# Performance work log

Hardware: AMD Instinct MI355X
Metric: run time of the kernel (lower is better)

Reference implementation:

```python
import jax, jax.numpy as jnp
import numpy as np

B, N, D, H = 128, 256, 256, 256
N_POWER_ITERS = 5  # matches spectral_norm(n_power_iterations=5)


def setup_inputs() -> dict:
    key = jax.random.key(0)
    ks = jax.random.split(key, 8)
    w = lambda k, shape: jax.random.normal(k, shape, dtype=jnp.float32) * 0.05
    return {
        "x": jax.random.normal(ks[0], (B, N, D), dtype=jnp.float32),
        "Wq": w(ks[1], (H, D)), "bq": w(ks[2], (H,)),
        "Wk": w(ks[3], (H, D)), "bk": w(ks[4], (H,)),
        "Wv": w(ks[5], (D, D)), "bv": w(ks[6], (D,)),
        "u0": jax.random.normal(ks[7], (D,), dtype=jnp.float32),
    }


def _l2norm(v, eps=1e-12):
    return v / (jnp.linalg.norm(v) + eps)


def _spectral_normalize(W, u0):
    # torch spectral_norm: power iteration (no grad) to get u, v; sigma = u^T W v (with grad)
    u = _l2norm(u0)
    v = _l2norm(W.T @ u)
    def body(i, uv):
        u, v = uv
        v = _l2norm(W.T @ u)
        u = _l2norm(W @ v)
        return (u, v)
    u, v = jax.lax.fori_loop(0, N_POWER_ITERS, body, (u, v))
    u = jax.lax.stop_gradient(u)
    v = jax.lax.stop_gradient(v)
    sigma = u @ (W @ v)
    return W / sigma


def reference(x, Wq, bq, Wk, bk, Wv, bv, u0):
    # torch Linear: y = x @ W.T + b, W is [out, in]
    q = jnp.einsum('bnd,hd->bnh', x, Wq) + bq          # [B, N, H]
    k = jnp.einsum('bnd,hd->bnh', x, Wk) + bk          # [B, N, H]
    Wv_sn = _spectral_normalize(Wv, u0)
    vals = jnp.einsum('bnd,od->bno', x, Wv_sn) + bv    # [B, N, D]
    scores = jnp.einsum('bnh,bmh->bnm', q, k)          # [B, N, N]
    # track_grads=False -> eigenvals detached; stop_gradient input so eig has no tangent path
    ev = jnp.linalg.eigvals(jax.lax.stop_gradient(scores))  # complex [B, N]
    rho = jnp.max(jnp.abs(ev), axis=-1)[:, None, None]      # spectral radius [B,1,1]
    attention = scores / rho
    weighted = jnp.einsum('bnm,bmd->bnd', attention, vals)  # [B, N, D]
    return weighted, attention
```

## Files before the change

kernel.cpp:

```cpp
#include <hip/hip_runtime.h>
#include <hip/hip_bf16.h>


#define NB 128
#define MAT 65536
#define BIG 8388608LL

typedef __attribute__((ext_vector_type(4))) float floatx4;
typedef __attribute__((ext_vector_type(4))) float f4v;
typedef __attribute__((ext_vector_type(8))) short short8v;
typedef __attribute__((ext_vector_type(4))) short short4v;

__device__ __forceinline__ short f2bf(float x) {
  union { float f; unsigned u; } v; v.f = x;
  unsigned r = v.u + 0x7fff + ((v.u >> 16) & 1);
  return (short)(r >> 16);
}
__device__ __forceinline__ float bf2f(short h) {
  union { unsigned u; float f; } v; v.u = ((unsigned)(unsigned short)h) << 16; return v.f;
}

template<bool TB, bool BATCHED>
__global__ __launch_bounds__(256) void gemm_mfma(
    const float* __restrict__ A, const float* __restrict__ B, float* __restrict__ C,
    long long sA, long long sB, long long sC,
    const float* __restrict__ bias,
    const float* __restrict__ scale_ptr, int sstride, int smode,
    float* __restrict__ norm_out,
    float* __restrict__ att_out,
    const float* __restrict__ B2, const float* __restrict__ bias2, float* __restrict__ C2,
    const float* __restrict__ B3, float* __restrict__ C3,
    const float* __restrict__ bsc, const float* __restrict__ bsb)
{
  __shared__ short sAhi[128 * 32], sAlo[128 * 32];
  __shared__ short sBhi[128 * 40], sBlo[128 * 40];

  int bz, m0, n0;
  if constexpr (BATCHED) {
    int lin = blockIdx.x;
    int xcd = lin & 7;
    int s = lin >> 3;
    bz = xcd * 16 + (s >> 2);
    int tile = s & 3;
    m0 = (tile >> 1) * 128;
    n0 = (tile & 1) * 128;
  } else {
    bz = 0;
    m0 = blockIdx.y * 128;
    n0 = (blockIdx.x & 1) * 128;
    int sel = blockIdx.x >> 1;
    if (sel == 1) { B = B2; bias = bias2; C = C2; }
    else if (sel == 2) { B = B3; bias = nullptr; C = C3; }
  }
  A += (long long)bz * sA;
  B += (long long)bz * sB;
  C += (long long)bz * sC;

  const int t = threadIdx.x;
  const int lane = t & 63;
  const int wave = t >> 6;
  const int wm = wave >> 1, wn = wave & 1;
  const int q = lane >> 4, c16 = lane & 15;

  float alpha = 1.0f;
  if (smode == 1) alpha = 1.0f / scale_ptr[bz * sstride];
  else if (smode == 2) alpha = scale_ptr[bz * sstride];

  float rinv_att = alpha;
  const bool do_att = (att_out != nullptr) && (n0 == 0);

  float binv = 1.0f;
  if (bsc) binv = 1.0f / bsc[0];

  floatx4 acc[4][4];
  #pragma unroll
  for (int i = 0; i < 4; i++)
    #pragma unroll
    for (int j = 0; j < 4; j++)
      acc[i][j] = (floatx4){0.f, 0.f, 0.f, 0.f};

  for (int k0 = 0; k0 < 256; k0 += 32) {
    #pragma unroll
    for (int i = 0; i < 4; i++) {
      int f = t + i * 256;
      int row = f >> 3, c4 = f & 7;
      f4v v = *(const f4v*)(A + (long long)(m0 + row) * 256 + k0 + c4 * 4);
      if (do_att)
        *(f4v*)(att_out + (long long)bz * MAT + (long long)(m0 + row) * 256 + k0 + c4 * 4)
            = v * rinv_att;
      short4v h, l;
      #pragma unroll
      for (int e = 0; e < 4; e++) {
        short hh = f2bf(v[e]);
        h[e] = hh;
        l[e] = f2bf(v[e] - bf2f(hh));
      }
      *(short4v*)&sAhi[row * 32 + c4 * 4] = h;
      *(short4v*)&sAlo[row * 32 + c4 * 4] = l;
    }
    if constexpr (TB) {
      #pragma unroll
      for (int i = 0; i < 4; i++) {
        int f = t + i * 256;
        int row = f >> 3, c4 = f & 7;
        f4v v = *(const f4v*)(B + (long long)(n0 + row) * 256 + k0 + c4 * 4);
        short4v h, l;
        #pragma unroll
        for (int e = 0; e < 4; e++) {
          short hh = f2bf(v[e]);
          h[e] = hh;
          l[e] = f2bf(v[e] - bf2f(hh));
        }
        *(short4v*)&sBhi[row * 40 + c4 * 4] = h;
        *(short4v*)&sBlo[row * 40 + c4 * 4] = l;
      }
      __syncthreads();
    } else {
      __shared__ float sT[32 * 132];
      #pragma unroll
      for (int i = 0; i < 4; i++) {
        int f = t + i * 256;
        int kk = f >> 5, n4 = f & 31;
        f4v v = *(const f4v*)(B + (long long)(k0 + kk) * 256 + n0 + n4 * 4);
        if (bsb) {
          #pragma unroll
          for (int e = 0; e < 4; e++) v[e] = v[e] * binv + bsb[n0 + n4 * 4 + e];
        }
        *(f4v*)&sT[kk * 132 + n4 * 4] = v;
      }
      __syncthreads();
      int n = t & 127, kh = t >> 7;
      short8v h0, h1, l0, l1;
      #pragma unroll
      for (int j = 0; j < 8; j++) {
        float x0 = sT[(kh * 16 + j) * 132 + n];
        float x1 = sT[(kh * 16 + 8 + j) * 132 + n];
        short a0 = f2bf(x0), a1 = f2bf(x1);
        h0[j] = a0; l0[j] = f2bf(x0 - bf2f(a0));
        h1[j] = a1; l1[j] = f2bf(x1 - bf2f(a1));
      }
      *(short8v*)&sBhi[n * 40 + kh * 16] = h0;
      *(short8v*)&sBhi[n * 40 + kh * 16 + 8] = h1;
      *(short8v*)&sBlo[n * 40 + kh * 16] = l0;
      *(short8v*)&sBlo[n * 40 + kh * 16 + 8] = l1;
      __syncthreads();
    }

    short8v ah[4], al[4], bh[4], bl[4];
    #pragma unroll
    for (int fi = 0; fi < 4; fi++) {
      int r = wm * 64 + fi * 16 + c16;
      ah[fi] = *(short8v*)&sAhi[r * 32 + q * 8];
      al[fi] = *(short8v*)&sAlo[r * 32 + q * 8];
    }
    #pragma unroll
    for (int fj = 0; fj < 4; fj++) {
      int r = wn * 64 + fj * 16 + c16;
      bh[fj] = *(short8v*)&sBhi[r * 40 + q * 8];
      bl[fj] = *(short8v*)&sBlo[r * 40 + q * 8];
    }
    #pragma unroll
    for (int fi = 0; fi < 4; fi++)
      #pragma unroll
      for (int fj = 0; fj < 4; fj++) {
        acc[fi][fj] = __builtin_amdgcn_mfma_f32_16x16x32_bf16(al[fi], bh[fj], acc[fi][fj], 0, 0, 0);
        acc[fi][fj] = __builtin_amdgcn_mfma_f32_16x16x32_bf16(ah[fi], bl[fj], acc[fi][fj], 0, 0, 0);
        acc[fi][fj] = __builtin_amdgcn_mfma_f32_16x16x32_bf16(ah[fi], bh[fj], acc[fi][fj], 0, 0, 0);
      }
    __syncthreads();
  }

  float ssq = 0.f;
  #pragma unroll
  for (int fi = 0; fi < 4; fi++) {
    #pragma unroll
    for (int fj = 0; fj < 4; fj++) {
      int col = n0 + wn * 64 + fj * 16 + c16;
      float bb = bias ? bias[col] : 0.f;
      #pragma unroll
      for (int r = 0; r < 4; r++) {
        int row = m0 + wm * 64 + fi * 16 + q * 4 + r;
        float v = acc[fi][fj][r] * alpha + bb;
        C[(long long)row * 256 + col] = v;
        ssq += v * v;
      }
    }
  }

  if (norm_out) {
    float* red = (float*)sAhi;
    red[t] = ssq;
    __syncthreads();
    for (int off = 128; off > 0; off >>= 1) {
      if (t < off) red[t] += red[t + off];
      __syncthreads();
    }
    if (t == 0) {
      int tl = ((m0 >> 7) << 1) | (n0 >> 7);
      norm_out[bz * 4 + tl] = red[0];
    }
  }
}

__global__ __launch_bounds__(256) void split_inputs(
    const float* __restrict__ Wq, const float* __restrict__ Wk,
    const float* __restrict__ Wv, short* __restrict__ ws6,
    const float* __restrict__ x, short* __restrict__ xhi, short* __restrict__ xlo)
{
  int b = blockIdx.x;
  int t = threadIdx.x;
  if (b < 192) {
    int gid = b * 256 + t;
    int m = gid >> 14;
    int off = (gid & 16383) * 4;
    const float* src = (m == 0) ? Wq : (m == 1) ? Wk : Wv;
    f4v v = *(const f4v*)(src + off);
    short4v h, l;
    #pragma unroll
    for (int e = 0; e < 4; e++) {
      short hh = f2bf(v[e]);
      h[e] = hh;
      l[e] = f2bf(v[e] - bf2f(hh));
    }
    *(short4v*)&ws6[(long long)(m * 2) * MAT + off] = h;
    *(short4v*)&ws6[(long long)(m * 2 + 1) * MAT + off] = l;
  } else {
    long long off = ((long long)(b - 192) * 256 + t) * 8;
    #pragma unroll
    for (int half = 0; half < 2; half++) {
      f4v v = *(const f4v*)(x + off + half * 4);
      short4v h, l;
      #pragma unroll
      for (int e = 0; e < 4; e++) {
        short hh = f2bf(v[e]);
        h[e] = hh;
        l[e] = f2bf(v[e] - bf2f(hh));
      }
      *(short4v*)&xhi[off + half * 4] = h;
      *(short4v*)&xlo[off + half * 4] = l;
    }
  }
}

__global__ __launch_bounds__(256) void proj_qkv(
    const short* __restrict__ xhi, const short* __restrict__ xlo,
    const short* __restrict__ wsp,
    const float* __restrict__ bq, const float* __restrict__ bk,
    short* __restrict__ qhi, short* __restrict__ qlo,
    short* __restrict__ khi, short* __restrict__ klo,
    float* __restrict__ vals)
{
  __shared__ short sAhi[128 * 32], sAlo[128 * 32];
  __shared__ short sBhi[128 * 40], sBlo[128 * 40];

  const int lin = blockIdx.x;
  const int xcd = lin & 7;
  const int idx = lin >> 3;
  const int mloc = idx / 6;
  const int s6 = idx - mloc * 6;
  const int m0 = (xcd * 32 + mloc) * 128;
  const int sel = s6 >> 1;
  const int n0 = (s6 & 1) * 128;

  const short* wb_hi = wsp + (long long)(sel * 2) * MAT;
  const short* wb_lo = wsp + (long long)(sel * 2 + 1) * MAT;

  const int t = threadIdx.x;
  const int lane = t & 63;
  const int wave = t >> 6;
  const int wm = wave >> 1, wn = wave & 1;
  const int q = lane >> 4, c16 = lane & 15;

  floatx4 acc[4][4];
  #pragma unroll
  for (int i = 0; i < 4; i++)
    #pragma unroll
    for (int j = 0; j < 4; j++)
      acc[i][j] = (floatx4){0.f, 0.f, 0.f, 0.f};

  for (int k0 = 0; k0 < 256; k0 += 32) {
    #pragma unroll
    for (int i = 0; i < 2; i++) {
      int chunk = t + i * 256;
      int row = chunk >> 2, c8 = chunk & 3;
      long long ga = (long long)(m0 + row) * 256 + k0 + c8 * 8;
      *(short8v*)&sAhi[row * 32 + c8 * 8] = *(const short8v*)(xhi + ga);
      *(short8v*)&sAlo[row * 32 + c8 * 8] = *(const short8v*)(xlo + ga);
    }
    #pragma unroll
    for (int i = 0; i < 2; i++) {
      int chunk = t + i * 256;
      int row = chunk >> 2, c8 = chunk & 3;
      long long gr = (long long)(n0 + row) * 256 + k0 + c8 * 8;
      *(short8v*)&sBhi[row * 40 + c8 * 8] = *(const short8v*)(wb_hi + gr);
      *(short8v*)&sBlo[row * 40 + c8 * 8] = *(const short8v*)(wb_lo + gr);
    }
    __syncthreads();

    short8v ah[4], al[4], bh[4], bl[4];
    #pragma unroll
    for (int fi = 0; fi < 4; fi++) {
      int r = wm * 64 + fi * 16 + c16;
      ah[fi] = *(short8v*)&sAhi[r * 32 + q * 8];
      al[fi] = *(short8v*)&sAlo[r * 32 + q * 8];
    }
    #pragma unroll
    for (int fj = 0; fj < 4; fj++) {
      int r = wn * 64 + fj * 16 + c16;
      bh[fj] = *(short8v*)&sBhi[r * 40 + q * 8];
      bl[fj] = *(short8v*)&sBlo[r * 40 + q * 8];
    }
    #pragma unroll
    for (int fi = 0; fi < 4; fi++)
      #pragma unroll
      for (int fj = 0; fj < 4; fj++) {
        acc[fi][fj] = __builtin_amdgcn_mfma_f32_16x16x32_bf16(al[fi], bh[fj], acc[fi][fj], 0, 0, 0);
        acc[fi][fj] = __builtin_amdgcn_mfma_f32_16x16x32_bf16(ah[fi], bl[fj], acc[fi][fj], 0, 0, 0);
        acc[fi][fj] = __builtin_amdgcn_mfma_f32_16x16x32_bf16(ah[fi], bh[fj], acc[fi][fj], 0, 0, 0);
      }
    __syncthreads();
  }

  if (sel < 2) {
    short* ohi = sel ? khi : qhi;
    short* olo = sel ? klo : qlo;
    const float* bb = sel ? bk : bq;
    #pragma unroll
    for (int fi = 0; fi < 4; fi++)
      #pragma unroll
      for (int fj = 0; fj < 4; fj++) {
        int col = n0 + wn * 64 + fj * 16 + c16;
        float b = bb[col];
        #pragma unroll
        for (int r = 0; r < 4; r++) {
          long long row = m0 + wm * 64 + fi * 16 + q * 4 + r;
          float v = acc[fi][fj][r] + b;
          short h = f2bf(v);
          ohi[row * 256 + col] = h;
          olo[row * 256 + col] = f2bf(v - bf2f(h));
        }
      }
  } else {
    #pragma unroll
    for (int fi = 0; fi < 4; fi++)
      #pragma unroll
      for (int fj = 0; fj < 4; fj++) {
        int col = n0 + wn * 64 + fj * 16 + c16;
        #pragma unroll
        for (int r = 0; r < 4; r++) {
          long long row = m0 + wm * 64 + fi * 16 + q * 4 + r;
          vals[row * 256 + col] = acc[fi][fj][r];
        }
      }
  }
}

__global__ __launch_bounds__(256) void scores_st(
    const short* __restrict__ qhi, const short* __restrict__ qlo,
    const short* __restrict__ khi, const short* __restrict__ klo,
    float* __restrict__ S, float* __restrict__ norm_out)
{
  __shared__ short sAhi[128 * 32], sAlo[128 * 32];
  __shared__ short sBhi[128 * 40], sBlo[128 * 40];
  __shared__ float red[256];

  const int lin = blockIdx.x;
  const int xcd = lin & 7, s = lin >> 3;
  const int bz = xcd * 16 + (s >> 2);
  const int tile = s & 3;
  const int m0 = (tile >> 1) * 128, n0 = (tile & 1) * 128;

  const int t = threadIdx.x;
  const int lane = t & 63;
  const int wave = t >> 6;
  const int wm = wave >> 1, wn = wave & 1;
  const int q = lane >> 4, c16 = lane & 15;

  floatx4 acc[4][4];
  #pragma unroll
  for (int i = 0; i < 4; i++)
    #pragma unroll
    for (int j = 0; j < 4; j++)
      acc[i][j] = (floatx4){0.f, 0.f, 0.f, 0.f};

  const long long abase = (long long)(bz * 256 + m0) * 256;
  const long long bbase = (long long)(bz * 256 + n0) * 256;

  for (int k0 = 0; k0 < 256; k0 += 32) {
    #pragma unroll
    for (int i = 0; i < 2; i++) {
      int chunk = t + i * 256;
      int row = chunk >> 2, c8 = chunk & 3;
      long long ga = abase + (long long)row * 256 + k0 + c8 * 8;
      long long gb = bbase + (long long)row * 256 + k0 + c8 * 8;
      *(short8v*)&sAhi[row * 32 + c8 * 8] = *(const short8v*)(qhi + ga);
      *(short8v*)&sAlo[row * 32 + c8 * 8] = *(const short8v*)(qlo + ga);
      *(short8v*)&sBhi[row * 40 + c8 * 8] = *(const short8v*)(khi + gb);
      *(short8v*)&sBlo[row * 40 + c8 * 8] = *(const short8v*)(klo + gb);
    }
    __syncthreads();

    short8v ah[4], al[4], bh[4], bl[4];
    #pragma unroll
    for (int fi = 0; fi < 4; fi++) {
      int r = wm * 64 + fi * 16 + c16;
      ah[fi] = *(short8v*)&sAhi[r * 32 + q * 8];
      al[fi] = *(short8v*)&sAlo[r * 32 + q * 8];
    }
    #pragma unroll
    for (int fj = 0; fj < 4; fj++) {
      int r = wn * 64 + fj * 16 + c16;
      bh[fj] = *(short8v*)&sBhi[r * 40 + q * 8];
      bl[fj] = *(short8v*)&sBlo[r * 40 + q * 8];
    }
    #pragma unroll
    for (int fi = 0; fi < 4; fi++)
      #pragma unroll
      for (int fj = 0; fj < 4; fj++) {
        acc[fi][fj] = __builtin_amdgcn_mfma_f32_16x16x32_bf16(al[fi], bh[fj], acc[fi][fj], 0, 0, 0);
        acc[fi][fj] = __builtin_amdgcn_mfma_f32_16x16x32_bf16(ah[fi], bl[fj], acc[fi][fj], 0, 0, 0);
        acc[fi][fj] = __builtin_amdgcn_mfma_f32_16x16x32_bf16(ah[fi], bh[fj], acc[fi][fj], 0, 0, 0);
      }
    __syncthreads();
  }

  float* C = S + (long long)bz * MAT;
  float ssq = 0.f;
  #pragma unroll
  for (int fi = 0; fi < 4; fi++)
    #pragma unroll
    for (int fj = 0; fj < 4; fj++) {
      int col = n0 + wn * 64 + fj * 16 + c16;
      #pragma unroll
      for (int r = 0; r < 4; r++) {
        int row = m0 + wm * 64 + fi * 16 + q * 4 + r;
        float v = acc[fi][fj][r];
        C[(long long)row * 256 + col] = v;
        ssq += v * v;
      }
    }

  red[t] = ssq;
  __syncthreads();
  for (int off = 128; off > 0; off >>= 1) {
    if (t < off) red[t] += red[t + off];
    __syncthreads();
  }
  if (t == 0) norm_out[bz * 4 + tile] = red[0];
}

__device__ __forceinline__ void chain_epilogue(
    short* LB, float* red, floatx4 (&acc)[4][4], float alpha,
    int m0, int n0, int wm, int wn, int q, int c16, int t,
    short* __restrict__ Mout,
    float* __restrict__ nout, int bz, int tile, bool write_out)
{
  __syncthreads();
  float ssq = 0.f;
  #pragma unroll
  for (int fi = 0; fi < 4; fi++)
    #pragma unroll
    for (int fj = 0; fj < 4; fj++) {
      int lcol = wn * 64 + fj * 16 + c16;
      #pragma unroll
      for (int r = 0; r < 4; r++) {
        int lrow = wm * 64 + fi * 16 + q * 4 + r;
        float v = acc[fi][fj][r] * alpha;
        ssq += v * v;
        if (write_out) LB[lrow * 128 + lcol] = f2bf(v);
      }
    }

  if (write_out) {
    __syncthreads();
    int lr = t >> 1, off = (t & 1) * 64;
    #pragma unroll
    for (int jc = 0; jc < 8; jc++)
      *(short8v*)(Mout + (long long)(m0 + lr) * 256 + n0 + off + jc * 8)
          = *(const short8v*)&LB[lr * 128 + off + jc * 8];
  }

  red[t] = ssq;
  __syncthreads();
  for (int off2 = 128; off2 > 0; off2 >>= 1) {
    if (t < off2) red[t] += red[t + off2];
    __syncthreads();
  }
  if (t == 0) nout[bz * 4 + tile] = red[0];
}

__global__ __launch_bounds__(256) void sq_f32bf(
    const float* __restrict__ S, short* __restrict__ Mo,
    const float* __restrict__ nprev, float* __restrict__ nout)
{
  __shared__ short SM[18432];
  __shared__ float sT[32 * 132];
  __shared__ float red[256];
  short* sAhi = SM;
  short* sAlo = SM + 4096;
  short* sBhi = SM + 8192;
  short* sBlo = SM + 13312;

  int lin = blockIdx.x;
  int xcd = lin & 7, s = lin >> 3;
  int bz = xcd * 16 + (s >> 2);
  int tile = s & 3;
  int m0 = (tile >> 1) * 128, n0 = (tile & 1) * 128;
  const float* A = S + (long long)bz * MAT;

  const int t = threadIdx.x;
  const int lane = t & 63;
  const int wave = t >> 6;
  const int wm = wave >> 1, wn = wave & 1;
  const int q = lane >> 4, c16 = lane & 15;

  floatx4 acc[4][4];
  #pragma unroll
  for (int i = 0; i < 4; i++)
    #pragma unroll
    for (int j = 0; j < 4; j++)
      acc[i][j] = (floatx4){0.f, 0.f, 0.f, 0.f};

  for (int k0 = 0; k0 < 256; k0 += 32) {
    #pragma unroll
    for (int i = 0; i < 4; i++) {
      int f = t + i * 256;
      int row = f >> 3, c4 = f & 7;
      f4v v = *(const f4v*)(A + (long long)(m0 + row) * 256 + k0 + c4 * 4);
      short4v h, l;
      #pragma unroll
      for (int e = 0; e < 4; e++) {
        short hh = f2bf(v[e]);
        h[e] = hh;
        l[e] = f2bf(v[e] - bf2f(hh));
      }
      *(short4v*)&sAhi[row * 32 + c4 * 4] = h;
      *(short4v*)&sAlo[row * 32 + c4 * 4] = l;
    }
    #pragma unroll
    for (int i = 0; i < 4; i++) {
      int f = t + i * 256;
      int kk = f >> 5, n4 = f & 31;
      f4v v = *(const f4v*)(A + (long long)(k0 + kk) * 256 + n0 + n4 * 4);
      *(f4v*)&sT[kk * 132 + n4 * 4] = v;
    }
    __syncthreads();
    {
      int n = t & 127, kh = t >> 7;
      short8v h0, h1, l0, l1;
      #pragma unroll
      for (int j = 0; j < 8; j++) {
        float x0 = sT[(kh * 16 + j) * 132 + n];
        float x1 = sT[(kh * 16 + 8 + j) * 132 + n];
        short a0 = f2bf(x0), a1 = f2bf(x1);
        h0[j] = a0; l0[j] = f2bf(x0 - bf2f(a0));
        h1[j] = a1; l1[j] = f2bf(x1 - bf2f(a1));
      }
      *(short8v*)&sBhi[n * 40 + kh * 16] = h0;
      *(short8v*)&sBhi[n * 40 + kh * 16 + 8] = h1;
      *(short8v*)&sBlo[n * 40 + kh * 16] = l0;
      *(short8v*)&sBlo[n * 40 + kh * 16 + 8] = l1;
    }
    __syncthreads();

    short8v ah[4], al[4], bh[4], bl[4];
    #pragma unroll
    for (int fi = 0; fi < 4; fi++) {
      int r = wm * 64 + fi * 16 + c16;
      ah[fi] = *(short8v*)&sAhi[r * 32 + q * 8];
      al[fi] = *(short8v*)&sAlo[r * 32 + q * 8];
    }
    #pragma unroll
    for (int fj = 0; fj < 4; fj++) {
      int r = wn * 64 + fj * 16 + c16;
      bh[fj] = *(short8v*)&sBhi[r * 40 + q * 8];
      bl[fj] = *(short8v*)&sBlo[r * 40 + q * 8];
    }
    #pragma unroll
    for (int fi = 0; fi < 4; fi++)
      #pragma unroll
      for (int fj = 0; fj < 4; fj++) {
        acc[fi][fj] = __builtin_amdgcn_mfma_f32_16x16x32_bf16(al[fi], bh[fj], acc[fi][fj], 0, 0, 0);
        acc[fi][fj] = __builtin_amdgcn_mfma_f32_16x16x32_bf16(ah[fi], bl[fj], acc[fi][fj], 0, 0, 0);
        acc[fi][fj] = __builtin_amdgcn_mfma_f32_16x16x32_bf16(ah[fi], bh[fj], acc[fi][fj], 0, 0, 0);
      }
    __syncthreads();
  }

  const float* p = nprev + bz * 4;
  float alpha = 1.0f / (p[0] + p[1] + p[2] + p[3]);
  chain_epilogue(SM, red, acc, alpha, m0, n0, wm, wn, q, c16, t,
                 Mo + (long long)bz * MAT, nout, bz, tile, true);
}

template<bool WRITE_OUT>
__global__ __launch_bounds__(256) void sq_bf(
    const short* __restrict__ Mi, short* __restrict__ Mo,
    const float* __restrict__ nprev, float* __restrict__ nout)
{
  __shared__ short SMEM[16384];
  __shared__ float red[256];
  short* BsA = SMEM;
  short* BsB = SMEM + 4608;

  int lin = blockIdx.x;
  int xcd = lin & 7, s = lin >> 3;
  int bz = xcd * 16 + (s >> 2);
  int tile = s & 3;
  int m0 = (tile >> 1) * 128, n0 = (tile & 1) * 128;

  const short* A = Mi + (long long)bz * MAT;

  const int t = threadIdx.x;
  const int lane = t & 63;
  const int wave = t >> 6;
  const int wm = wave >> 1, wn = wave & 1;
  const int q = lane >> 4, c16 = lane & 15;
  const int g = t >> 5, cc = t & 31;

  floatx4 acc[4][4];
  #pragma unroll
  for (int i = 0; i < 4; i++)
    #pragma unroll
    for (int j = 0; j < 4; j++)
      acc[i][j] = (floatx4){0.f, 0.f, 0.f, 0.f};

  short4v r0 = *(const short4v*)(A + (long long)(g * 4 + 0) * 256 + n0 + cc * 4);
  short4v r1 = *(const short4v*)(A + (long long)(g * 4 + 1) * 256 + n0 + cc * 4);
  short4v r2 = *(const short4v*)(A + (long long)(g * 4 + 2) * 256 + n0 + cc * 4);
  short4v r3 = *(const short4v*)(A + (long long)(g * 4 + 3) * 256 + n0 + cc * 4);

  for (int k0 = 0; k0 < 256; k0 += 32) {
    short* Bw = ((k0 >> 5) & 1) ? BsB : BsA;
    #pragma unroll
    for (int j = 0; j < 4; j++) {
      short4v w4 = (short4v){r0[j], r1[j], r2[j], r3[j]};
      *(short4v*)&Bw[(cc * 4 + j) * 36 + g * 4] = w4;
    }
    __syncthreads();

    if (k0 < 224) {
      int kn = k0 + 32;
      r0 = *(const short4v*)(A + (long long)(kn + g * 4 + 0) * 256 + n0 + cc * 4);
      r1 = *(const short4v*)(A + (long long)(kn + g * 4 + 1) * 256 + n0 + cc * 4);
      r2 = *(const short4v*)(A + (long long)(kn + g * 4 + 2) * 256 + n0 + cc * 4);
      r3 = *(const short4v*)(A + (long long)(kn + g * 4 + 3) * 256 + n0 + cc * 4);
    }

    short8v a[4], b[4];
    #pragma unroll
    for (int fi = 0; fi < 4; fi++)
      a[fi] = *(const short8v*)(A + (long long)(m0 + wm * 64 + fi * 16 + c16) * 256 + k0 + q * 8);
    #pragma unroll
    for (int fj = 0; fj < 4; fj++) {
      int n = wn * 64 + fj * 16 + c16;
      short4v lo = *(const short4v*)&Bw[n * 36 + q * 8];
      short4v hi = *(const short4v*)&Bw[n * 36 + q * 8 + 4];
      b[fj] = __builtin_shufflevector(lo, hi, 0, 1, 2, 3, 4, 5, 6, 7);
    }
    #pragma unroll
    for (int fi = 0; fi < 4; fi++)
      #pragma unroll
      for (int fj = 0; fj < 4; fj++)
        acc[fi][fj] = __builtin_amdgcn_mfma_f32_16x16x32_bf16(a[fi], b[fj], acc[fi][fj], 0, 0, 0);
  }

  const float* p = nprev + bz * 4;
  float alpha = 1.0f / (p[0] + p[1] + p[2] + p[3]);
  chain_epilogue(SMEM, red, acc, alpha, m0, n0, wm, wn, q, c16, t,
                 WRITE_OUT ? Mo + (long long)bz * MAT : nullptr,
                 nout, bz, tile, WRITE_OUT);
}

__global__ __launch_bounds__(128) void rho_finalize(
    const float* __restrict__ partials, float* __restrict__ rho_inv)
{
  int bz = threadIdx.x;
  float a2 = 0.f, w = 1.0f;
  #pragma unroll
  for (int i2 = 0; i2 <= 12; i2++) {
    const float* p = partials + i2 * 512 + bz * 4;
    a2 += w * 0.5f * logf(p[0] + p[1] + p[2] + p[3]);
    w *= 0.5f;
  }
  rho_inv[bz] = expf(-a2);
}

__device__ __forceinline__ float bsum1024(float x, float* red, int t)
{
  red[t] = x; __syncthreads();
  for (int off = 512; off > 0; off >>= 1) {
    if (t < off) red[t] += red[t + off];
    __syncthreads();
  }
  float r = red[0];
  __syncthreads();
  return r;
}

__global__ __launch_bounds__(1024) void sigma_kernel(
    const float* __restrict__ W, const float* __restrict__ u0, float* __restrict__ sigma)
{
  __shared__ short Wl[65536];
  __shared__ float u[256], v[256], red[1024];
  int t = threadIdx.x;
  int r = t & 255, seg = t >> 8;
  const float eps = 1e-12f;

  #pragma unroll
  for (int i = 0; i < 16; i++) {
    int idx = (i * 1024 + t) * 4;
    f4v w = *(const f4v*)(W + idx);
    short4v h;
    #pragma unroll
    for (int e = 0; e < 4; e++) h[e] = f2bf(w[e]);
    *(short4v*)&Wl[idx] = h;
  }

  float x = (t < 256) ? u0[t] : 0.f;
  float nrm = sqrtf(bsum1024(x * x, red, t));
  if (t < 256) u[t] = x / (nrm + eps);
  __syncthreads();

  for (int it = 0; it < 5; it++) {
    float sv = 0.f;
    #pragma unroll 8
    for (int j = 0; j < 64; j++) {
      int h = seg * 64 + j;
      sv = fmaf(bf2f(Wl[h * 256 + r]), u[h], sv);
    }
    red[t] = sv; __syncthreads();
    float vr = 0.f;
    if (t < 256) vr = red[t] + red[256 + t] + red[512 + t] + red[768 + t];
    __syncthreads();
    nrm = sqrtf(bsum1024(t < 256 ? vr * vr : 0.f, red, t));
    if (t < 256) v[t] = vr / (nrm + eps);
    __syncthreads();
    if (it < 4) {
      float su = 0.f;
      #pragma unroll
      for (int j = 0; j < 16; j++) {
        short4v w4 = *(const short4v*)&Wl[r * 256 + seg * 64 + j * 4];
        const float* vv = &v[seg * 64 + j * 4];
        su += bf2f(w4[0]) * vv[0] + bf2f(w4[1]) * vv[1]
            + bf2f(w4[2]) * vv[2] + bf2f(w4[3]) * vv[3];
      }
      red[t] = su; __syncthreads();
      float ur = 0.f;
      if (t < 256) ur = red[t] + red[256 + t] + red[512 + t] + red[768 + t];
      __syncthreads();
      nrm = sqrtf(bsum1024(t < 256 ? ur * ur : 0.f, red, t));
      if (t < 256) u[t] = ur / (nrm + eps);
      __syncthreads();
    }
  }

  float z = 0.f;
  #pragma unroll
  for (int j = 0; j < 16; j++) {
    f4v w = *(const f4v*)(W + r * 256 + seg * 64 + j * 4);
    const float* vv = &v[seg * 64 + j * 4];
    z += w[0] * vv[0] + w[1] * vv[1] + w[2] * vv[2] + w[3] * vv[3];
  }
  red[t] = z; __syncthreads();
  float zr = 0.f;
  if (t < 256) zr = red[t] + red[256 + t] + red[512 + t] + red[768 + t];
  __syncthreads();
  float zz = bsum1024(t < 256 ? zr * zr : 0.f, red, t);
  if (t == 0) sigma[0] = sqrtf(zz);
}

extern "C" void kernel_launch(void* const* d_in, const int* in_sizes, int n_in,
                              void* d_out, int out_size, void* d_ws, size_t ws_size,
                              hipStream_t stream)
{
  const float* x  = (const float*)d_in[0];
  const float* Wq = (const float*)d_in[1];
  const float* bq = (const float*)d_in[2];
  const float* Wk = (const float*)d_in[3];
  const float* bk = (const float*)d_in[4];
  const float* Wv = (const float*)d_in[5];
  const float* bv = (const float*)d_in[6];
  const float* u0 = (const float*)d_in[7];

  float* out  = (float*)d_out;
  float* out0 = out;
  float* out1 = out + BIG;
  short* out0s = (short*)out0;
  short* out1s = (short*)out1;

  short* qhi = out0s;
  short* qlo = out0s + 32768LL * 256;
  short* khi = out1s;
  short* klo = out1s + 32768LL * 256;

  float* ws         = (float*)d_ws;
  float* scores_buf = ws;
  float* vals_buf   = ws + BIG;
  float* partials   = ws + 2 * BIG;
  float* sigma      = partials + 13 * 512;
  float* rho_inv    = sigma + 4;
  short* wsplit     = (short*)(rho_inv + 128);

  short* xhi = (short*)scores_buf;
  short* xlo = xhi + BIG;

  dim3 blk(256);

  split_inputs<<<dim3(4288, 1, 1), blk, 0, stream>>>(Wq, Wk, Wv, wsplit, x, xhi, xlo);

  proj_qkv<<<dim3(1536, 1, 1), blk, 0, stream>>>(
      xhi, xlo, wsplit, bq, bk, qhi, qlo, khi, klo, vals_buf);

  scores_st<<<dim3(512, 1, 1), blk, 0, stream>>>(
      qhi, qlo, khi, klo, scores_buf, partials);

  sigma_kernel<<<1, dim3(1024), 0, stream>>>(Wv, u0, sigma);

  sq_f32bf<<<dim3(512, 1, 1), blk, 0, stream>>>(scores_buf, out0s, partials, partials + 512);

  const short* cin = out0s;
  for (int i = 0; i < 10; i++) {
    short* cout = (i & 1) ? out0s : out1s;
    sq_bf<true><<<dim3(512, 1, 1), blk, 0, stream>>>(cin, cout,
        partials + (1 + i) * 512, partials + (2 + i) * 512);
    cin = cout;
  }
  sq_bf<false><<<dim3(512, 1, 1), blk, 0, stream>>>(cin, nullptr,
      partials + 11 * 512, partials + 12 * 512);

  rho_finalize<<<1, dim3(128), 0, stream>>>(partials, rho_inv);

  gemm_mfma<false, true><<<dim3(512, 1, 1), blk, 0, stream>>>(
      scores_buf, vals_buf, out0, MAT, MAT, MAT, nullptr, rho_inv, 1, 2, nullptr,
      out1, nullptr, nullptr, nullptr, nullptr, nullptr, sigma, bv);
}
```

Measured before the change: 479.3 us.

## Store scores as pre-split bf16 hi/lo pairs and stage epilogue writes through LDS

The scores kernel now writes its result as two bf16 planes (hi and lo) instead of fp32. The first squaring kernel and the final attention GEMM read these planes directly, so they no longer repeat the fp32-to-bf16 split on load. The projection and scores epilogues stage each tile in shared memory so global stores become coalesced 16-byte row writes instead of scattered 2- and 4-byte stores. The generic gemm_mfma kernel is replaced by a dedicated final_gemm. The attention output is rebuilt from hi+lo, which is a slightly lossy approximation of the fp32 scores.

```diff
diff --git a/kernel.cpp b/kernel.cpp
--- a/kernel.cpp
+++ b/kernel.cpp
@@ -18,188 +18,6 @@
 }
 __device__ __forceinline__ float bf2f(short h) {
   union { unsigned u; float f; } v; v.u = ((unsigned)(unsigned short)h) << 16; return v.f;
-}
-
-template<bool TB, bool BATCHED>
-__global__ __launch_bounds__(256) void gemm_mfma(
-    const float* __restrict__ A, const float* __restrict__ B, float* __restrict__ C,
-    long long sA, long long sB, long long sC,
-    const float* __restrict__ bias,
-    const float* __restrict__ scale_ptr, int sstride, int smode,
-    float* __restrict__ norm_out,
-    float* __restrict__ att_out,
-    const float* __restrict__ B2, const float* __restrict__ bias2, float* __restrict__ C2,
-    const float* __restrict__ B3, float* __restrict__ C3,
-    const float* __restrict__ bsc, const float* __restrict__ bsb)
-{
-  __shared__ short sAhi[128 * 32], sAlo[128 * 32];
-  __shared__ short sBhi[128 * 40], sBlo[128 * 40];
-
-  int bz, m0, n0;
-  if constexpr (BATCHED) {
-    int lin = blockIdx.x;
-    int xcd = lin & 7;
-    int s = lin >> 3;
-    bz = xcd * 16 + (s >> 2);
-    int tile = s & 3;
-    m0 = (tile >> 1) * 128;
-    n0 = (tile & 1) * 128;
-  } else {
-    bz = 0;
-    m0 = blockIdx.y * 128;
-    n0 = (blockIdx.x & 1) * 128;
-    int sel = blockIdx.x >> 1;
-    if (sel == 1) { B = B2; bias = bias2; C = C2; }
-    else if (sel == 2) { B = B3; bias = nullptr; C = C3; }
-  }
-  A += (long long)bz * sA;
-  B += (long long)bz * sB;
-  C += (long long)bz * sC;
-
-  const int t = threadIdx.x;
-  const int lane = t & 63;
-  const int wave = t >> 6;
-  const int wm = wave >> 1, wn = wave & 1;
-  const int q = lane >> 4, c16 = lane & 15;
-
-  float alpha = 1.0f;
-  if (smode == 1) alpha = 1.0f / scale_ptr[bz * sstride];
-  else if (smode == 2) alpha = scale_ptr[bz * sstride];
-
-  float rinv_att = alpha;
-  const bool do_att = (att_out != nullptr) && (n0 == 0);
-
-  float binv = 1.0f;
-  if (bsc) binv = 1.0f / bsc[0];
-
-  floatx4 acc[4][4];
-  #pragma unroll
-  for (int i = 0; i < 4; i++)
-    #pragma unroll
-    for (int j = 0; j < 4; j++)
-      acc[i][j] = (floatx4){0.f, 0.f, 0.f, 0.f};
-
-  for (int k0 = 0; k0 < 256; k0 += 32) {
-    #pragma unroll
-    for (int i = 0; i < 4; i++) {
-      int f = t + i * 256;
-      int row = f >> 3, c4 = f & 7;
-      f4v v = *(const f4v*)(A + (long long)(m0 + row) * 256 + k0 + c4 * 4);
-      if (do_att)
-        *(f4v*)(att_out + (long long)bz * MAT + (long long)(m0 + row) * 256 + k0 + c4 * 4)
-            = v * rinv_att;
-      short4v h, l;
-      #pragma unroll
-      for (int e = 0; e < 4; e++) {
-        short hh = f2bf(v[e]);
-        h[e] = hh;
-        l[e] = f2bf(v[e] - bf2f(hh));
-      }
-      *(short4v*)&sAhi[row * 32 + c4 * 4] = h;
-      *(short4v*)&sAlo[row * 32 + c4 * 4] = l;
-    }
-    if constexpr (TB) {
-      #pragma unroll
-      for (int i = 0; i < 4; i++) {
-        int f = t + i * 256;
-        int row = f >> 3, c4 = f & 7;
-        f4v v = *(const f4v*)(B + (long long)(n0 + row) * 256 + k0 + c4 * 4);
-        short4v h, l;
-        #pragma unroll
-        for (int e = 0; e < 4; e++) {
-          short hh = f2bf(v[e]);
-          h[e] = hh;
-          l[e] = f2bf(v[e] - bf2f(hh));
-        }
-        *(short4v*)&sBhi[row * 40 + c4 * 4] = h;
-        *(short4v*)&sBlo[row * 40 + c4 * 4] = l;
-      }
-      __syncthreads();
-    } else {
-      __shared__ float sT[32 * 132];
-      #pragma unroll
-      for (int i = 0; i < 4; i++) {
-        int f = t + i * 256;
-        int kk = f >> 5, n4 = f & 31;
-        f4v v = *(const f4v*)(B + (long long)(k0 + kk) * 256 + n0 + n4 * 4);
-        if (bsb) {
-          #pragma unroll
-          for (int e = 0; e < 4; e++) v[e] = v[e] * binv + bsb[n0 + n4 * 4 + e];
-        }
-        *(f4v*)&sT[kk * 132 + n4 * 4] = v;
-      }
-      __syncthreads();
-      int n = t & 127, kh = t >> 7;
-      short8v h0, h1, l0, l1;
-      #pragma unroll
-      for (int j = 0; j < 8; j++) {
-        float x0 = sT[(kh * 16 + j) * 132 + n];
-        float x1 = sT[(kh * 16 + 8 + j) * 132 + n];
-        short a0 = f2bf(x0), a1 = f2bf(x1);
-        h0[j] = a0; l0[j] = f2bf(x0 - bf2f(a0));
-        h1[j] = a1; l1[j] = f2bf(x1 - bf2f(a1));
-      }
-      *(short8v*)&sBhi[n * 40 + kh * 16] = h0;
-      *(short8v*)&sBhi[n * 40 + kh * 16 + 8] = h1;
-      *(short8v*)&sBlo[n * 40 + kh * 16] = l0;
-      *(short8v*)&sBlo[n * 40 + kh * 16 + 8] = l1;
-      __syncthreads();
-    }
-
-    short8v ah[4], al[4], bh[4], bl[4];
-    #pragma unroll
-    for (int fi = 0; fi < 4; fi++) {
-      int r = wm * 64 + fi * 16 + c16;
-      ah[fi] = *(short8v*)&sAhi[r * 32 + q * 8];
-      al[fi] = *(short8v*)&sAlo[r * 32 + q * 8];
-    }
-    #pragma unroll
-    for (int fj = 0; fj < 4; fj++) {
-      int r = wn * 64 + fj * 16 + c16;
-      bh[fj] = *(short8v*)&sBhi[r * 40 + q * 8];
-      bl[fj] = *(short8v*)&sBlo[r * 40 + q * 8];
-    }
-    #pragma unroll
-    for (int fi = 0; fi < 4; fi++)
-      #pragma unroll
-      for (int fj = 0; fj < 4; fj++) {
-        acc[fi][fj] = __builtin_amdgcn_mfma_f32_16x16x32_bf16(al[fi], bh[fj], acc[fi][fj], 0, 0, 0);
-        acc[fi][fj] = __builtin_amdgcn_mfma_f32_16x16x32_bf16(ah[fi], bl[fj], acc[fi][fj], 0, 0, 0);
-        acc[fi][fj] = __builtin_amdgcn_mfma_f32_16x16x32_bf16(ah[fi], bh[fj], acc[fi][fj], 0, 0, 0);
-      }
-    __syncthreads();
-  }
-
-  float ssq = 0.f;
-  #pragma unroll
-  for (int fi = 0; fi < 4; fi++) {
-    #pragma unroll
-    for (int fj = 0; fj < 4; fj++) {
-      int col = n0 + wn * 64 + fj * 16 + c16;
-      float bb = bias ? bias[col] : 0.f;
-      #pragma unroll
-      for (int r = 0; r < 4; r++) {
-        int row = m0 + wm * 64 + fi * 16 + q * 4 + r;
-        float v = acc[fi][fj][r] * alpha + bb;
-        C[(long long)row * 256 + col] = v;
-        ssq += v * v;
-      }
-    }
-  }
-
-  if (norm_out) {
-    float* red = (float*)sAhi;
-    red[t] = ssq;
-    __syncthreads();
-    for (int off = 128; off > 0; off >>= 1) {
-      if (t < off) red[t] += red[t + off];
-      __syncthreads();
-    }
-    if (t == 0) {
-      int tl = ((m0 >> 7) << 1) | (n0 >> 7);
-      norm_out[bz * 4 + tl] = red[0];
-    }
-  }
 }
 
 __global__ __launch_bounds__(256) void split_inputs(
@@ -250,8 +68,11 @@
     short* __restrict__ khi, short* __restrict__ klo,
     float* __restrict__ vals)
 {
-  __shared__ short sAhi[128 * 32], sAlo[128 * 32];
-  __shared__ short sBhi[128 * 40], sBlo[128 * 40];
+  __shared__ short SM[18432];
+  short* sAhi = SM;
+  short* sAlo = SM + 4096;
+  short* sBhi = SM + 8192;
+  short* sBlo = SM + 13312;
 
   const int lin = blockIdx.x;
   const int xcd = lin & 7;
@@ -325,21 +146,46 @@
     short* ohi = sel ? khi : qhi;
     short* olo = sel ? klo : qlo;
     const float* bb = sel ? bk : bq;
+    short* LB = SM;
+    const int lr = t >> 1, off = (t & 1) * 64;
+
     #pragma unroll
     for (int fi = 0; fi < 4; fi++)
       #pragma unroll
       for (int fj = 0; fj < 4; fj++) {
-        int col = n0 + wn * 64 + fj * 16 + c16;
-        float b = bb[col];
+        int lcol = wn * 64 + fj * 16 + c16;
+        float b = bb[n0 + lcol];
         #pragma unroll
         for (int r = 0; r < 4; r++) {
-          long long row = m0 + wm * 64 + fi * 16 + q * 4 + r;
+          int lrow = wm * 64 + fi * 16 + q * 4 + r;
+          LB[lrow * 128 + lcol] = f2bf(acc[fi][fj][r] + b);
+        }
+      }
+    __syncthreads();
+    #pragma unroll
+    for (int jc = 0; jc < 8; jc++)
+      *(short8v*)(ohi + (long long)(m0 + lr) * 256 + n0 + off + jc * 8)
+          = *(const short8v*)&LB[lr * 128 + off + jc * 8];
+    __syncthreads();
+
+    #pragma unroll
+    for (int fi = 0; fi < 4; fi++)
+      #pragma unroll
+      for (int fj = 0; fj < 4; fj++) {
+        int lcol = wn * 64 + fj * 16 + c16;
+        float b = bb[n0 + lcol];
+        #pragma unroll
+        for (int r = 0; r < 4; r++) {
+          int lrow = wm * 64 + fi * 16 + q * 4 + r;
           float v = acc[fi][fj][r] + b;
-          short h = f2bf(v);
-          ohi[row * 256 + col] = h;
-          olo[row * 256 + col] = f2bf(v - bf2f(h));
+          LB[lrow * 128 + lcol] = f2bf(v - bf2f(f2bf(v)));
         }
       }
+    __syncthreads();
+    #pragma unroll
+    for (int jc = 0; jc < 8; jc++)
+      *(short8v*)(olo + (long long)(m0 + lr) * 256 + n0 + off + jc * 8)
+          = *(const short8v*)&LB[lr * 128 + off + jc * 8];
   } else {
     #pragma unroll
     for (int fi = 0; fi < 4; fi++)
@@ -358,11 +204,15 @@
 __global__ __launch_bounds__(256) void scores_st(
     const short* __restrict__ qhi, const short* __restrict__ qlo,
     const short* __restrict__ khi, const short* __restrict__ klo,
-    float* __restrict__ S, float* __restrict__ norm_out)
-{
-  __shared__ short sAhi[128 * 32], sAlo[128 * 32];
-  __shared__ short sBhi[128 * 40], sBlo[128 * 40];
+    short* __restrict__ Shi, short* __restrict__ Slo,
+    float* __restrict__ norm_out)
+{
+  __shared__ short SM[18432];
   __shared__ float red[256];
+  short* sAhi = SM;
+  short* sAlo = SM + 4096;
+  short* sBhi = SM + 8192;
+  short* sBlo = SM + 13312;
 
   const int lin = blockIdx.x;
   const int xcd = lin & 7, s = lin >> 3;
@@ -424,26 +274,52 @@
     __syncthreads();
   }
 
-  float* C = S + (long long)bz * MAT;
+  short* LB = SM;
+  const int lr = t >> 1, off = (t & 1) * 64;
   float ssq = 0.f;
+
   #pragma unroll
   for (int fi = 0; fi < 4; fi++)
     #pragma unroll
     for (int fj = 0; fj < 4; fj++) {
-      int col = n0 + wn * 64 + fj * 16 + c16;
+      int lcol = wn * 64 + fj * 16 + c16;
       #pragma unroll
       for (int r = 0; r < 4; r++) {
-        int row = m0 + wm * 64 + fi * 16 + q * 4 + r;
+        int lrow = wm * 64 + fi * 16 + q * 4 + r;
         float v = acc[fi][fj][r];
-        C[(long long)row * 256 + col] = v;
         ssq += v * v;
-      }
-    }
+        LB[lrow * 128 + lcol] = f2bf(v);
+      }
+    }
+  __syncthreads();
+  #pragma unroll
+  for (int jc = 0; jc < 8; jc++)
+    *(short8v*)(Shi + (long long)bz * MAT + (long long)(m0 + lr) * 256 + n0 + off + jc * 8)
+        = *(const short8v*)&LB[lr * 128 + off + jc * 8];
+  __syncthreads();
+
+  #pragma unroll
+  for (int fi = 0; fi < 4; fi++)
+    #pragma unroll
+    for (int fj = 0; fj < 4; fj++) {
+      int lcol = wn * 64 + fj * 16 + c16;
+      #pragma unroll
+      for (int r = 0; r < 4; r++) {
+        int lrow = wm * 64 + fi * 16 + q * 4 + r;
+        float v = acc[fi][fj][r];
+        LB[lrow * 128 + lcol] = f2bf(v - bf2f(f2bf(v)));
+      }
+    }
+  __syncthreads();
+  #pragma unroll
+  for (int jc = 0; jc < 8; jc++)
+    *(short8v*)(Slo + (long long)bz * MAT + (long long)(m0 + lr) * 256 + n0 + off + jc * 8)
+        = *(const short8v*)&LB[lr * 128 + off + jc * 8];
 
   red[t] = ssq;
   __syncthreads();
-  for (int off = 128; off > 0; off >>= 1) {
-    if (t < off) red[t] += red[t + off];
+  for (int o = 128; o > 0; o >>= 1) {
+    if (t < o) red[t] += red[t + o];
     __syncthreads();
   }
   if (t == 0) norm_out[bz * 4 + tile] = red[0];
@@ -489,30 +365,31 @@
   if (t == 0) nout[bz * 4 + tile] = red[0];
 }
 
-__global__ __launch_bounds__(256) void sq_f32bf(
-    const float* __restrict__ S, short* __restrict__ Mo,
+__global__ __launch_bounds__(256) void sq_split(
+    const short* __restrict__ Shi, const short* __restrict__ Slo,
+    short* __restrict__ Mo,
     const float* __restrict__ nprev, float* __restrict__ nout)
 {
-  __shared__ short SM[18432];
-  __shared__ float sT[32 * 132];
+  __shared__ short SMEM[16384];
   __shared__ float red[256];
-  short* sAhi = SM;
-  short* sAlo = SM + 4096;
-  short* sBhi = SM + 8192;
-  short* sBlo = SM + 13312;
+  short* Bsh = SMEM;
+  short* Bsl = SMEM + 4608;
 
   int lin = blockIdx.x;
   int xcd = lin & 7, s = lin >> 3;
   int bz = xcd * 16 + (s >> 2);
   int tile = s & 3;
   int m0 = (tile >> 1) * 128, n0 = (tile & 1) * 128;
-  const float* A = S + (long long)bz * MAT;
+
+  const short* Ah = Shi + (long long)bz * MAT;
+  const short* Al = Slo + (long long)bz * MAT;
 
   const int t = threadIdx.x;
   const int lane = t & 63;
   const int wave = t >> 6;
   const int wm = wave >> 1, wn = wave & 1;
   const int q = lane >> 4, c16 = lane & 15;
+  const int g = t >> 5, cc = t & 31;
 
   floatx4 acc[4][4];
   #pragma unroll
@@ -522,26 +399,215 @@
       acc[i][j] = (floatx4){0.f, 0.f, 0.f, 0.f};
 
   for (int k0 = 0; k0 < 256; k0 += 32) {
-    #pragma unroll
-    for (int i = 0; i < 4; i++) {
-      int f = t + i * 256;
-      int row = f >> 3, c4 = f & 7;
-      f4v v = *(const f4v*)(A + (long long)(m0 + row) * 256 + k0 + c4 * 4);
-      short4v h, l;
-      #pragma unroll
-      for (int e = 0; e < 4; e++) {
-        short hh = f2bf(v[e]);
-        h[e] = hh;
-        l[e] = f2bf(v[e] - bf2f(hh));
-      }
-      *(short4v*)&sAhi[row * 32 + c4 * 4] = h;
-      *(short4v*)&sAlo[row * 32 + c4 * 4] = l;
+    __syncthreads();
+    short4v h0 = *(const short4v*)(Ah + (long long)(k0 + g * 4 + 0) * 256 + n0 + cc * 4);
+    short4v h1 = *(const short4v*)(Ah + (long long)(k0 + g * 4 + 1) * 256 + n0 + cc * 4);
+    short4v h2 = *(const short4v*)(Ah + (long long)(k0 + g * 4 + 2) * 256 + n0 + cc * 4);
+    short4v h3 = *(const short4v*)(Ah + (long long)(k0 + g * 4 + 3) * 256 + n0 + cc * 4);
+    short4v l0 = *(const short4v*)(Al + (long long)(k0 + g * 4 + 0) * 256 + n0 + cc * 4);
+    short4v l1 = *(const short4v*)(Al + (long long)(k0 + g * 4 + 1) * 256 + n0 + cc * 4);
+    short4v l2 = *(const short4v*)(Al + (long long)(k0 + g * 4 + 2) * 256 + n0 + cc * 4);
+    short4v l3 = *(const short4v*)(Al + (long long)(k0 + g * 4 + 3) * 256 + n0 + cc * 4);
+    #pragma unroll
+    for (int j = 0; j < 4; j++) {
+      *(short4v*)&Bsh[(cc * 4 + j) * 36 + g * 4] = (short4v){h0[j], h1[j], h2[j], h3[j]};
+      *(short4v*)&Bsl[(cc * 4 + j) * 36 + g * 4] = (short4v){l0[j], l1[j], l2[j], l3[j]};
+    }
+    __syncthreads();
+
+    short8v ah[4], al[4], bh[4], bl[4];
+    #pragma unroll
+    for (int fi = 0; fi < 4; fi++) {
+      long long r = (long long)(m0 + wm * 64 + fi * 16 + c16) * 256 + k0 + q * 8;
+      ah[fi] = *(const short8v*)(Ah + r);
+      al[fi] = *(const short8v*)(Al + r);
+    }
+    #pragma unroll
+    for (int fj = 0; fj < 4; fj++) {
+      int n = wn * 64 + fj * 16 + c16;
+      short4v hlo = *(const short4v*)&Bsh[n * 36 + q * 8];
+      short4v hhi = *(const short4v*)&Bsh[n * 36 + q * 8 + 4];
+      short4v llo = *(const short4v*)&Bsl[n * 36 + q * 8];
+      short4v lhi = *(const short4v*)&Bsl[n * 36 + q * 8 + 4];
+      bh[fj] = __builtin_shufflevector(hlo, hhi, 0, 1, 2, 3, 4, 5, 6, 7);
+      bl[fj] = __builtin_shufflevector(llo, lhi, 0, 1, 2, 3, 4, 5, 6, 7);
+    }
+    #pragma unroll
+    for (int fi = 0; fi < 4; fi++)
+      #pragma unroll
+      for (int fj = 0; fj < 4; fj++) {
+        acc[fi][fj] = __builtin_amdgcn_mfma_f32_16x16x32_bf16(al[fi], bh[fj], acc[fi][fj], 0, 0, 0);
+        acc[fi][fj] = __builtin_amdgcn_mfma_f32_16x16x32_bf16(ah[fi], bl[fj], acc[fi][fj], 0, 0, 0);
+        acc[fi][fj] = __builtin_amdgcn_mfma_f32_16x16x32_bf16(ah[fi], bh[fj], acc[fi][fj], 0, 0, 0);
+      }
+  }
+
+  const float* p = nprev + bz * 4;
+  float alpha = 1.0f / (p[0] + p[1] + p[2] + p[3]);
+  chain_epilogue(SMEM, red, acc, alpha, m0, n0, wm, wn, q, c16, t,
+                 Mo + (long long)bz * MAT, nout, bz, tile, true);
+}
+
+template<bool WRITE_OUT>
+__global__ __launch_bounds__(256) void sq_bf(
+    const short* __restrict__ Mi, short* __restrict__ Mo,
+    const float* __restrict__ nprev, float* __restrict__ nout)
+{
+  __shared__ short SMEM[16384];
+  __shared__ float red[256];
+  short* BsA = SMEM;
+  short* BsB = SMEM + 4608;
+
+  int lin = blockIdx.x;
+  int xcd = lin & 7, s = lin >> 3;
+  int bz = xcd * 16 + (s >> 2);
+  int tile = s & 3;
+  int m0 = (tile >> 1) * 128, n0 = (tile & 1) * 128;
+
+  const short* A = Mi + (long long)bz * MAT;
+
+  const int t = threadIdx.x;
+  const int lane = t & 63;
+  const int wave = t >> 6;
+  const int wm = wave >> 1, wn = wave & 1;
+  const int q = lane >> 4, c16 = lane & 15;
+  const int g = t >> 5, cc = t & 31;
+
+  floatx4 acc[4][4];
+  #pragma unroll
+  for (int i = 0; i < 4; i++)
+    #pragma unroll
+    for (int j = 0; j < 4; j++)
+      acc[i][j] = (floatx4){0.f, 0.f, 0.f, 0.f};
+
+  short4v r0 = *(const short4v*)(A + (long long)(g * 4 + 0) * 256 + n0 + cc * 4);
+  short4v r1 = *(const short4v*)(A + (long long)(g * 4 + 1) * 256 + n0 + cc * 4);
+  short4v r2 = *(const short4v*)(A + (long long)(g * 4 + 2) * 256 + n0 + cc * 4);
+  short4v r3 = *(const short4v*)(A + (long long)(g * 4 + 3) * 256 + n0 + cc * 4);
+
+  for (int k0 = 0; k0 < 256; k0 += 32) {
+    short* Bw = ((k0 >> 5) & 1) ? BsB : BsA;
+    #pragma unroll
+    for (int j = 0; j < 4; j++) {
+      short4v w4 = (short4v){r0[j], r1[j], r2[j], r3[j]};
+      *(short4v*)&Bw[(cc * 4 + j) * 36 + g * 4] = w4;
+    }
+    __syncthreads();
+
+    if (k0 < 224) {
+      int kn = k0 + 32;
+      r0 = *(const short4v*)(A + (long long)(kn + g * 4 + 0) * 256 + n0 + cc * 4);
+      r1 = *(const short4v*)(A + (long long)(kn + g * 4 + 1) * 256 + n0 + cc * 4);
+      r2 = *(const short4v*)(A + (long long)(kn + g * 4 + 2) * 256 + n0 + cc * 4);
+      r3 = *(const short4v*)(A + (long long)(kn + g * 4 + 3) * 256 + n0 + cc * 4);
+    }
+
+    short8v a[4], b[4];
+    #pragma unroll
+    for (int fi = 0; fi < 4; fi++)
+      a[fi] = *(const short8v*)(A + (long long)(m0 + wm * 64 + fi * 16 + c16) * 256 + k0 + q * 8);
+    #pragma unroll
+    for (int fj = 0; fj < 4; fj++) {
+      int n = wn * 64 + fj * 16 + c16;
+      short4v lo = *(const short4v*)&Bw[n * 36 + q * 8];
+      short4v hi = *(const short4v*)&Bw[n * 36 + q * 8 + 4];
+      b[fj] = __builtin_shufflevector(lo, hi, 0, 1, 2, 3, 4, 5, 6, 7);
+    }
+    #pragma unroll
+    for (int fi = 0; fi < 4; fi++)
+      #pragma unroll
+      for (int fj = 0; fj < 4; fj++)
+        acc[fi][fj] = __builtin_amdgcn_mfma_f32_16x16x32_bf16(a[fi], b[fj], acc[fi][fj], 0, 0, 0);
+  }
+
+  const float* p = nprev + bz * 4;
+  float alpha = 1.0f / (p[0] + p[1] + p[2] + p[3]);
+  chain_epilogue(SMEM, red, acc, alpha, m0, n0, wm, wn, q, c16, t,
+                 WRITE_OUT ? Mo + (long long)bz * MAT : nullptr,
+                 nout, bz, tile, WRITE_OUT);
+}
+
+__global__ __launch_bounds__(128) void rho_finalize(
+    const float* __restrict__ partials, float* __restrict__ rho_inv)
+{
+  int bz = threadIdx.x;
+  float a2 = 0.f, w = 1.0f;
+  #pragma unroll
+  for (int i2 = 0; i2 <= 12; i2++) {
+    const float* p = partials + i2 * 512 + bz * 4;
+    a2 += w * 0.5f * logf(p[0] + p[1] + p[2] + p[3]);
+    w *= 0.5f;
+  }
+  rho_inv[bz] = expf(-a2);
+}
+
+__global__ __launch_bounds__(256) void final_gemm(
+    const short* __restrict__ Shi, const short* __restrict__ Slo,
+    const float* __restrict__ Bv, float* __restrict__ C,
+    float* __restrict__ att_out,
+    const float* __restrict__ rho_inv, const float* __restrict__ sigma,
+    const float* __restrict__ bv)
+{
+  __shared__ short sAhi[128 * 32], sAlo[128 * 32];
+  __shared__ short sBhi[128 * 40], sBlo[128 * 40];
+  __shared__ float sT[32 * 132];
+
+  const int lin = blockIdx.x;
+  const int xcd = lin & 7, s = lin >> 3;
+  const int bz = xcd * 16 + (s >> 2);
+  const int tile = s & 3;
+  const int m0 = (tile >> 1) * 128, n0 = (tile & 1) * 128;
+
+  const int t = threadIdx.x;
+  const int lane = t & 63;
+  const int wave = t >> 6;
+  const int wm = wave >> 1, wn = wave & 1;
+  const int q = lane >> 4, c16 = lane & 15;
+
+  const float alpha = rho_inv[bz];
+  const float binv = 1.0f / sigma[0];
+  const bool do_att = (n0 == 0);
+
+  const short* Ah = Shi + (long long)bz * MAT;
+  const short* Al = Slo + (long long)bz * MAT;
+  const float* B = Bv + (long long)bz * MAT;
+  float* Cb = C + (long long)bz * MAT;
+  float* attb = att_out + (long long)bz * MAT;
+
+  floatx4 acc[4][4];
+  #pragma unroll
+  for (int i = 0; i < 4; i++)
+    #pragma unroll
+    for (int j = 0; j < 4; j++)
+      acc[i][j] = (floatx4){0.f, 0.f, 0.f, 0.f};
+
+  for (int k0 = 0; k0 < 256; k0 += 32) {
+    #pragma unroll
+    for (int i = 0; i < 2; i++) {
+      int chunk = t + i * 256;
+      int row = chunk >> 2, c8 = chunk & 3;
+      long long ga = (long long)(m0 + row) * 256 + k0 + c8 * 8;
+      short8v h8 = *(const short8v*)(Ah + ga);
+      short8v l8 = *(const short8v*)(Al + ga);
+      *(short8v*)&sAhi[row * 32 + c8 * 8] = h8;
+      *(short8v*)&sAlo[row * 32 + c8 * 8] = l8;
+      if (do_att) {
+        f4v o0, o1;
+        #pragma unroll
+        for (int j = 0; j < 4; j++) o0[j] = (bf2f(h8[j]) + bf2f(l8[j])) * alpha;
+        #pragma unroll
+        for (int j = 0; j < 4; j++) o1[j] = (bf2f(h8[4 + j]) + bf2f(l8[4 + j])) * alpha;
+        *(f4v*)(attb + ga) = o0;
+        *(f4v*)(attb + ga + 4) = o1;
+      }
     }
     #pragma unroll
     for (int i = 0; i < 4; i++) {
       int f = t + i * 256;
       int kk = f >> 5, n4 = f & 31;
-      f4v v = *(const f4v*)(A + (long long)(k0 + kk) * 256 + n0 + n4 * 4);
+      f4v v = *(const f4v*)(B + (long long)(k0 + kk) * 256 + n0 + n4 * 4);
+      #pragma unroll
+      for (int e = 0; e < 4; e++) v[e] = v[e] * binv + bv[n0 + n4 * 4 + e];
       *(f4v*)&sT[kk * 132 + n4 * 4] = v;
     }
     __syncthreads();
@@ -587,103 +653,17 @@
     __syncthreads();
   }
 
-  const float* p = nprev + bz * 4;
-  float alpha = 1.0f / (p[0] + p[1] + p[2] + p[3]);
-  chain_epilogue(SM, red, acc, alpha, m0, n0, wm, wn, q, c16, t,
-                 Mo + (long long)bz * MAT, nout, bz, tile, true);
-}
-
-template<bool WRITE_OUT>
-__global__ __launch_bounds__(256) void sq_bf(
-    const short* __restrict__ Mi, short* __restrict__ Mo,
-    const float* __restrict__ nprev, float* __restrict__ nout)
-{
-  __shared__ short SMEM[16384];
-  __shared__ float red[256];
-  short* BsA = SMEM;
-  short* BsB = SMEM + 4608;
-
-  int lin = blockIdx.x;
-  int xcd = lin & 7, s = lin >> 3;
-  int bz = xcd * 16 + (s >> 2);
-  int tile = s & 3;
-  int m0 = (tile >> 1) * 128, n0 = (tile & 1) * 128;
-
-  const short* A = Mi + (long long)bz * MAT;
-
-  const int t = threadIdx.x;
-  const int lane = t & 63;
-  const int wave = t >> 6;
-  const int wm = wave >> 1, wn = wave & 1;
-  const int q = lane >> 4, c16 = lane & 15;
-  const int g = t >> 5, cc = t & 31;
-
-  floatx4 acc[4][4];
-  #pragma unroll
-  for (int i = 0; i < 4; i++)
-    #pragma unroll
-    for (int j = 0; j < 4; j++)
-      acc[i][j] = (floatx4){0.f, 0.f, 0.f, 0.f};
-
-  short4v r0 = *(const short4v*)(A + (long long)(g * 4 + 0) * 256 + n0 + cc * 4);
-  short4v r1 = *(const short4v*)(A + (long long)(g * 4 + 1) * 256 + n0 + cc * 4);
-  short4v r2 = *(const short4v*)(A + (long long)(g * 4 + 2) * 256 + n0 + cc * 4);
-  short4v r3 = *(const short4v*)(A + (long long)(g * 4 + 3) * 256 + n0 + cc * 4);
-
-  for (int k0 = 0; k0 < 256; k0 += 32) {
-    short* Bw = ((k0 >> 5) & 1) ? BsB : BsA;
-    #pragma unroll
-    for (int j = 0; j < 4; j++) {
-      short4v w4 = (short4v){r0[j], r1[j], r2[j], r3[j]};
-      *(short4v*)&Bw[(cc * 4 + j) * 36 + g * 4] = w4;
-    }
-    __syncthreads();
-
-    if (k0 < 224) {
-      int kn = k0 + 32;
-      r0 = *(const short4v*)(A + (long long)(kn + g * 4 + 0) * 256 + n0 + cc * 4);
-      r1 = *(const short4v*)(A + (long long)(kn + g * 4 + 1) * 256 + n0 + cc * 4);
-      r2 = *(const short4v*)(A + (long long)(kn + g * 4 + 2) * 256 + n0 + cc * 4);
-      r3 = *(const short4v*)(A + (long long)(kn + g * 4 + 3) * 256 + n0 + cc * 4);
-    }
-
-    short8v a[4], b[4];
-    #pragma unroll
-    for (int fi = 0; fi < 4; fi++)
-      a[fi] = *(const short8v*)(A + (long long)(m0 + wm * 64 + fi * 16 + c16) * 256 + k0 + q * 8);
+  #pragma unroll
+  for (int fi = 0; fi < 4; fi++)
     #pragma unroll
     for (int fj = 0; fj < 4; fj++) {
-      int n = wn * 64 + fj * 16 + c16;
-      short4v lo = *(const short4v*)&Bw[n * 36 + q * 8];
-      short4v hi = *(const short4v*)&Bw[n * 36 + q * 8 + 4];
-      b[fj] = __builtin_shufflevector(lo, hi, 0, 1, 2, 3, 4, 5, 6, 7);
-    }
-    #pragma unroll
-    for (int fi = 0; fi < 4; fi++)
-      #pragma unroll
-      for (int fj = 0; fj < 4; fj++)
-        acc[fi][fj] = __builtin_amdgcn_mfma_f32_16x16x32_bf16(a[fi], b[fj], acc[fi][fj], 0, 0, 0);
-  }
-
-  const float* p = nprev + bz * 4;
-  float alpha = 1.0f / (p[0] + p[1] + p[2] + p[3]);
-  chain_epilogue(SMEM, red, acc, alpha, m0, n0, wm, wn, q, c16, t,
-                 WRITE_OUT ? Mo + (long long)bz * MAT : nullptr,
-                 nout, bz, tile, WRITE_OUT);
-}
-
-__global__ __launch_bounds__(128) void rho_finalize(
-    const float* __restrict__ partials, float* __restrict__ rho_inv)
-{
-  int bz = threadIdx.x;
-  float a2 = 0.f, w = 1.0f;
-  #pragma unroll
-  for (int i2 = 0; i2 <= 12; i2++) {
-    const float* p = partials + i2 * 512 + bz * 4;
-    a2 += w * 0.5f * logf(p[0] + p[1] + p[2] + p[3]);
-    w *= 0.5f;
-  }
-  rho_inv[bz] = expf(-a2);
+      int col = n0 + wn * 64 + fj * 16 + c16;
+      #pragma unroll
+      for (int r = 0; r < 4; r++) {
+        int row = m0 + wm * 64 + fi * 16 + q * 4 + r;
+        Cb[(long long)row * 256 + col] = acc[fi][fj][r] * alpha;
+      }
+    }
 }
 
 __device__ __forceinline__ float bsum1024(float x, float* red, int t)
@@ -804,6 +784,8 @@
 
   short* xhi = (short*)scores_buf;
   short* xlo = xhi + BIG;
+  short* Shi = (short*)scores_buf;
+  short* Slo = Shi + BIG;
 
   dim3 blk(256);
 
@@ -813,11 +795,11 @@
       xhi, xlo, wsplit, bq, bk, qhi, qlo, khi, klo, vals_buf);
 
   scores_st<<<dim3(512, 1, 1), blk, 0, stream>>>(
-      qhi, qlo, khi, klo, scores_buf, partials);
+      qhi, qlo, khi, klo, Shi, Slo, partials);
 
   sigma_kernel<<<1, dim3(1024), 0, stream>>>(Wv, u0, sigma);
 
-  sq_f32bf<<<dim3(512, 1, 1), blk, 0, stream>>>(scores_buf, out0s, partials, partials + 512);
+  sq_split<<<dim3(512, 1, 1), blk, 0, stream>>>(Shi, Slo, out0s, partials, partials + 512);
 
   const short* cin = out0s;
   for (int i = 0; i < 10; i++) {
@@ -831,7 +813,6 @@
 
   rho_finalize<<<1, dim3(128), 0, stream>>>(partials, rho_inv);
 
-  gemm_mfma<false, true><<<dim3(512, 1, 1), blk, 0, stream>>>(
-      scores_buf, vals_buf, out0, MAT, MAT, MAT, nullptr, rho_inv, 1, 2, nullptr,
-      out1, nullptr, nullptr, nullptr, nullptr, nullptr, sigma, bv);
-}
+  final_gemm<<<dim3(512, 1, 1), blk, 0, stream>>>(
+      Shi, Slo, vals_buf, out0, out1, rho_inv, sigma, bv);
+}
```

After: 503.4 us. 1.05x slower.
